# Kernel tuning notes

Hardware: AMD Instinct MI355X
Metric: run time of the kernel (lower is better)

The kernel has to match this reference:

```python
import jax, jax.numpy as jnp
import numpy as np

THRESHOLD = 0.5
SLACK = 3
EPS = 1e-12
B, H, W = 16, 512, 512


def _shift(p, dy, dx, b, h, w):
    # p is zero-padded by 1 on spatial dims; returns neighbor at offset (dy, dx)
    return p[:, 1 + dy:1 + dy + h, 1 + dx:1 + dx + w]


def _thin_sub(img, step):
    # One Zhang-Suen sub-iteration on bool image [B,H,W] (zero boundary, as skimage)
    b, h, w = img.shape
    p = jnp.pad(img.astype(jnp.int32), ((0, 0), (1, 1), (1, 1)))
    # P2..P9 clockwise starting at North
    P2 = _shift(p, -1, 0, b, h, w); P3 = _shift(p, -1, 1, b, h, w)
    P4 = _shift(p, 0, 1, b, h, w);  P5 = _shift(p, 1, 1, b, h, w)
    P6 = _shift(p, 1, 0, b, h, w);  P7 = _shift(p, 1, -1, b, h, w)
    P8 = _shift(p, 0, -1, b, h, w); P9 = _shift(p, -1, -1, b, h, w)
    seq = [P2, P3, P4, P5, P6, P7, P8, P9, P2]
    Bn = P2 + P3 + P4 + P5 + P6 + P7 + P8 + P9          # neighbor count
    A = sum((1 - seq[k]) * seq[k + 1] for k in range(8))  # 0->1 transitions
    cond = (Bn >= 2) & (Bn <= 6) & (A == 1)
    if step == 0:
        cond = cond & (P2 * P4 * P6 == 0) & (P4 * P6 * P8 == 0)
    else:
        cond = cond & (P2 * P4 * P8 == 0) & (P2 * P6 * P8 == 0)
    return img & ~cond


def _skeletonize(img):
    # Iterate Zhang-Suen thinning to convergence (skimage.morphology.skeletonize 2D = Zhang's method)
    def body(state):
        cur, _ = state
        nxt = _thin_sub(_thin_sub(cur, 0), 1)
        return (nxt, jnp.any(nxt != cur))

    out, _ = jax.lax.while_loop(lambda s: s[1], body, (img, jnp.array(True)))
    return out


def _edt_sq(mask):
    # Exact squared Euclidean distance to nearest True pixel, separable 2-pass.
    b, h, w = mask.shape
    BIG = h + w  # larger than any attainable 1D distance
    g = jnp.where(mask, 0, BIG).astype(jnp.int32)  # [B,H,W]

    # pass 1: 1D nearest-True distance along rows (axis=1) via fwd/bwd scans
    def fscan(carry, row):
        d = jnp.minimum(row, carry + 1)
        return d, d

    g_rows = jnp.moveaxis(g, 1, 0)  # [H,B,W]
    init = jnp.full((b, w), BIG, jnp.int32)
    _, fwd = jax.lax.scan(fscan, init, g_rows)
    _, bwd = jax.lax.scan(fscan, init, g_rows[::-1])
    f = jnp.minimum(jnp.minimum(fwd, bwd[::-1]), BIG)  # [H,B,W]
    f2 = jnp.moveaxis(f * f, 0, 1)  # [B,H,W] squared vertical distance

    # pass 2: d2[b,i,j] = min_{j'} f2[b,i,j'] + (j-j')^2 (lower envelope, memory-friendly lax.map)
    js = jnp.arange(w, dtype=jnp.int32)

    def one_col(j):
        off = (js - j) ** 2  # [W]
        return jnp.min(f2 + off[None, None, :], axis=-1)  # [B,H]

    d2 = jax.lax.map(one_col, js)  # [W,B,H]
    return jnp.transpose(d2, (1, 2, 0))  # [B,H,W]


def setup_inputs() -> dict:
    key = jax.random.key(0)
    k1, k2 = jax.random.split(key)
    y_pred = jax.random.uniform(k1, (B, H, W), dtype=jnp.float32)
    y_true = jax.random.uniform(k2, (B, H, W), dtype=jnp.float32)
    return {"y_pred": y_pred, "y_true": y_true}


def reference(y_pred, y_true):
    p = y_pred > THRESHOLD  # greater_is_road=True binarization
    g = y_true > THRESHOLD
    p = _skeletonize(p)
    g = _skeletonize(g)
    d2_gt = _edt_sq(g)   # EDT of ~g == distance to nearest g pixel
    d2_pr = _edt_sq(p)
    s2 = SLACK * SLACK   # dist <= slack  <=>  dist^2 <= slack^2 (integer sq EDT)
    tp_area = d2_gt <= s2
    fp_area = ~tp_area
    fn_area = d2_pr > s2
    ax = (1, 2)
    TP = jnp.sum(tp_area & p, ax).astype(jnp.float32)
    FP = jnp.sum(fp_area & p, ax).astype(jnp.float32)
    FN = jnp.sum(fn_area & g, ax).astype(jnp.float32)
    correctness = TP / (TP + FP + EPS)
    completeness = TP / (TP + FN + EPS)
    quality = TP / (TP + FP + FN + EPS)
    # mean over batch -> [3]: [correctness, completeness, quality]
    return jnp.mean(jnp.stack([correctness, completeness, quality], axis=1), axis=0)
```

## Files before the change

kernel.cpp:

```cpp
#include <hip/hip_runtime.h>
#include <stdint.h>

#define HH 512
#define WW 512
#define HW (HH * WW)
#define WPR 8
#define NWORDS (HH * WPR)
#define NTHREADS 1024
#define NB 16
#define NIMG (2 * NB)

#define LSTR 10
#define LROWS (HH + 2)
#define LWORDS (LROWS * LSTR)

typedef unsigned long long u64;

__device__ __forceinline__ u64 zs_core(u64 cc, u64 P2, u64 P3, u64 P4, u64 P5,
                                       u64 P6, u64 P7, u64 P8, u64 P9, int step) {
    u64 ab = P2 ^ P3;
    u64 s1 = ab ^ P4, c1 = (P2 & P3) | (ab & P4);
    u64 de = P5 ^ P6;
    u64 s2 = de ^ P7, c2 = (P5 & P6) | (de & P7);
    u64 s3 = P8 ^ P9, c3 = P8 & P9;
    u64 gh = s1 ^ s2;
    u64 b0 = gh ^ s3, c4 = (s1 & s2) | (gh & s3);
    u64 ij = c1 ^ c2;
    u64 s4 = ij ^ c3, c5 = (c1 & c2) | (ij & c3);
    u64 b1 = s4 ^ c4, c6 = s4 & c4;
    u64 b2 = c5 ^ c6, b3 = c5 & c6;

    u64 Bge2 = b1 | b2 | b3;
    u64 Ble6 = ~(b3 | (b2 & b1 & b0));

    u64 a1, a2, t;
    t = ~P2 & P3; a1 = t; a2 = 0ULL;
    t = ~P3 & P4; a2 |= a1 & t; a1 |= t;
    t = ~P4 & P5; a2 |= a1 & t; a1 |= t;
    t = ~P5 & P6; a2 |= a1 & t; a1 |= t;
    t = ~P6 & P7; a2 |= a1 & t; a1 |= t;
    t = ~P7 & P8; a2 |= a1 & t; a1 |= t;
    t = ~P8 & P9; a2 |= a1 & t; a1 |= t;
    t = ~P9 & P2; a2 |= a1 & t; a1 |= t;
    u64 Aeq1 = a1 & ~a2;

    u64 sccond = (step == 0) ? ~((P4 & P6) & (P2 | P8))
                             : ~((P2 & P8) & (P4 | P6));

    return cc & ~(Bge2 & Ble6 & Aeq1 & sccond);
}

__global__ __launch_bounds__(256)
void pack_kernel(const float* __restrict__ y_pred,
                 const float* __restrict__ y_true,
                 u64* __restrict__ bits ,
                 int* __restrict__ cnt ) {
    int tid = threadIdx.x;
    if (blockIdx.x == 0 && tid < 4 * NB + NIMG + 1) cnt[tid] = 0;

    int t = blockIdx.x * 256 + tid;
    size_t g0 = (size_t)t * 16;
    const float* src;
    size_t off;
    if (g0 < (size_t)NB * HW) { src = y_pred; off = g0; }
    else                      { src = y_true; off = g0 - (size_t)NB * HW; }
    const float4* s4 = (const float4*)(src + off);
    float4 a = s4[0];
    float4 b = s4[1];
    float4 c = s4[2];
    float4 d = s4[3];
    unsigned m =
        ((unsigned)(a.x > 0.5f) << 0)  | ((unsigned)(a.y > 0.5f) << 1)  |
        ((unsigned)(a.z > 0.5f) << 2)  | ((unsigned)(a.w > 0.5f) << 3)  |
        ((unsigned)(b.x > 0.5f) << 4)  | ((unsigned)(b.y > 0.5f) << 5)  |
        ((unsigned)(b.z > 0.5f) << 6)  | ((unsigned)(b.w > 0.5f) << 7)  |
        ((unsigned)(c.x > 0.5f) << 8)  | ((unsigned)(c.y > 0.5f) << 9)  |
        ((unsigned)(c.z > 0.5f) << 10) | ((unsigned)(c.w > 0.5f) << 11) |
        ((unsigned)(d.x > 0.5f) << 12) | ((unsigned)(d.y > 0.5f) << 13) |
        ((unsigned)(d.z > 0.5f) << 14) | ((unsigned)(d.w > 0.5f) << 15);
    ((unsigned short*)bits)[t] = (unsigned short)m;
}

#define SSTRIPS 8
#define SIROWS (HH / SSTRIPS)
#define SHALO 24
#define SDROWS (SIROWS + 2 * SHALO)
#define STHREADS (SDROWS * WPR)
#define SITERS (SHALO / 2)
#define SSTR 10
#define SLWORDS ((SDROWS + 2) * SSTR)

__global__ __launch_bounds__(STHREADS)
void strip_kernel(const u64* __restrict__ src, u64* __restrict__ dst,
                  int* __restrict__ flags, int rec) {
    __shared__ u64 Mb[2][SLWORDS];
    __shared__ int s_any[3];

    int bx = blockIdx.x;
    int img = bx >> 3;
    int s = bx & 7;
    int tid = threadIdx.x;
    int lane = tid & 63;
    int r = tid >> 3;
    int c = tid & 7;
    int gr = s * SIROWS - SHALO + r;

    for (int i = tid; i < SLWORDS; i += STHREADS) { Mb[0][i] = 0; Mb[1][i] = 0; }
    if (tid < 3) s_any[tid] = 0;
    __syncthreads();

    const u64* gsrc = src + (size_t)img * NWORDS;
    u64 v = (gr >= 0 && gr < HH) ? gsrc[gr * WPR + c] : 0ULL;
    int base = (r + 1) * SSTR + (c + 1);
    Mb[0][base] = v;

    bool prevchg = true;
    int it = 0;
    bool done = false;
    for (;;) {
        for (int step = 0; step < 2; ++step) {
            __syncthreads();
            if (step == 0 && it > 0) {
                if (s_any[(it + 2) % 3] == 0) { done = true; break; }
            }
            const u64* Ms = Mb[step];
            u64* Md = Mb[step ^ 1];
            u64 cc = Ms[base];
            u64 nv = cc;
            bool chg = false;
            if (cc) {
                u64 nm = Ms[base - SSTR - 1], nc = Ms[base - SSTR], np = Ms[base - SSTR + 1];
                u64 cm = Ms[base - 1],                              cp = Ms[base + 1];
                u64 sm = Ms[base + SSTR - 1], sc = Ms[base + SSTR], sp = Ms[base + SSTR + 1];
                u64 P2 = nc;
                u64 P3 = (nc >> 1) | (np << 63);
                u64 P4 = (cc >> 1) | (cp << 63);
                u64 P5 = (sc >> 1) | (sp << 63);
                u64 P6 = sc;
                u64 P7 = (sc << 1) | (sm >> 63);
                u64 P8 = (cc << 1) | (cm >> 63);
                u64 P9 = (nc << 1) | (nm >> 63);
                nv = zs_core(cc, P2, P3, P4, P5, P6, P7, P8, P9, step);
                chg = (nv != cc);
            }
            if (chg | prevchg) Md[base] = nv;
            prevchg = chg;
            u64 bal = __ballot(chg);
            if (bal && lane == 0) s_any[it % 3] = 1;
            if (step == 1 && tid == 0) s_any[(it + 1) % 3] = 0;
        }
        if (done) break;
        if (++it >= SITERS) break;
    }
    __syncthreads();
    int lastAny = done ? 0 : s_any[(SITERS - 1) % 3];

    if (r >= SHALO && r < SHALO + SIROWS) {
        dst[(size_t)img * NWORDS + gr * WPR + c] = Mb[0][base];
    }
    if (rec && lastAny && tid == 0) flags[img] = 1;
}

__global__ __launch_bounds__(NTHREADS, 4)
void skel_kernel(u64* __restrict__ bits, const int* __restrict__ flags) {
    __shared__ u64 Mb[2][LWORDS];
    __shared__ unsigned int Cpb[2][130];
    __shared__ int s_any[3];

    int bx = blockIdx.x;
    if (flags[bx] == 0) return;

    int tid = threadIdx.x;
    int lane = tid & 63;
    int c = tid & 7;
    int rb = tid >> 3;

    u64* gm = bits + (size_t)bx * NWORDS;

    if (tid < LROWS) {
        int i = tid;
        if (i == 0 || i == LROWS - 1) {
            #pragma unroll
            for (int j = 0; j < LSTR; ++j) { Mb[0][i * LSTR + j] = 0; Mb[1][i * LSTR + j] = 0; }
        } else {
            Mb[0][i * LSTR + 0] = 0; Mb[0][i * LSTR + 9] = 0;
            Mb[1][i * LSTR + 0] = 0; Mb[1][i * LSTR + 9] = 0;
        }
    }
    {
        const ulonglong2* s2 = (const ulonglong2*)gm;
        #pragma unroll
        for (int k = 0; k < 2; ++k) {
            int i = k * NTHREADS + tid;
            ulonglong2 v = s2[i];
            int wi = i * 2;
            int r = wi >> 3, c2 = wi & 7;
            int li = (r + 1) * LSTR + c2 + 1;
            Mb[0][li] = v.x;
            Mb[0][li + 1] = v.y;
        }
    }
    if (tid < 130) {
        Cpb[0][tid] = (tid >= 1 && tid <= 128) ? 0x1FEu : 0u;
        Cpb[1][tid] = 0u;
    }
    if (tid < 3) s_any[tid] = 0;

    unsigned dl = 0x1FEu;
    bool prevchg = true;
    int base = (rb * 4 + 1) * LSTR + (c + 1);

    int it = 0;
    bool done = false;
    for (;;) {
        for (int step = 0; step < 2; ++step) {
            __syncthreads();
            if (step == 0 && it > 0) {
                if (s_any[(it + 2) % 3] == 0) { done = true; break; }
            }
            const u64* Ms = Mb[step];
            u64* Md = Mb[step ^ 1];
            const unsigned* CpS = Cpb[step];
            unsigned* CpD = Cpb[step ^ 1];

            unsigned need = ((CpS[rb] | CpS[rb + 1] | CpS[rb + 2]) >> c) & 7u;
            bool chg = false;
            if (need) {
                u64 Ca, Ea, Wa, Cb, Eb, Wb, Cc, Ec, Wc;
                {   int a = base - LSTR;
                    u64 x = Ms[a], mm = Ms[a - 1], pp = Ms[a + 1];
                    Ca = x; Ea = (x >> 1) | (pp << 63); Wa = (x << 1) | (mm >> 63); }
                {   int a = base;
                    u64 x = Ms[a], mm = Ms[a - 1], pp = Ms[a + 1];
                    Cb = x; Eb = (x >> 1) | (pp << 63); Wb = (x << 1) | (mm >> 63); }
                u64 nv0 = 0, nv1 = 0, nv2 = 0, nv3 = 0;
                {   int a = base + LSTR;
                    u64 x = Ms[a], mm = Ms[a - 1], pp = Ms[a + 1];
                    Cc = x; Ec = (x >> 1) | (pp << 63); Wc = (x << 1) | (mm >> 63);
                    if (Cb) nv0 = zs_core(Cb, Ca, Ea, Eb, Ec, Cc, Wc, Wb, Wa, step);
                    chg |= (nv0 != Cb);
                    Ca = Cb; Ea = Eb; Wa = Wb; Cb = Cc; Eb = Ec; Wb = Wc; }
                {   int a = base + 2 * LSTR;
                    u64 x = Ms[a], mm = Ms[a - 1], pp = Ms[a + 1];
                    Cc = x; Ec = (x >> 1) | (pp << 63); Wc = (x << 1) | (mm >> 63);
                    if (Cb) nv1 = zs_core(Cb, Ca, Ea, Eb, Ec, Cc, Wc, Wb, Wa, step);
                    chg |= (nv1 != Cb);
                    Ca = Cb; Ea = Eb; Wa = Wb; Cb = Cc; Eb = Ec; Wb = Wc; }
                {   int a = base + 3 * LSTR;
                    u64 x = Ms[a], mm = Ms[a - 1], pp = Ms[a + 1];
                    Cc = x; Ec = (x >> 1) | (pp << 63); Wc = (x << 1) | (mm >> 63);
                    if (Cb) nv2 = zs_core(Cb, Ca, Ea, Eb, Ec, Cc, Wc, Wb, Wa, step);
                    chg |= (nv2 != Cb);
                    Ca = Cb; Ea = Eb; Wa = Wb; Cb = Cc; Eb = Ec; Wb = Wc; }
                {   int a = base + 4 * LSTR;
                    u64 x = Ms[a], mm = Ms[a - 1], pp = Ms[a + 1];
                    Cc = x; Ec = (x >> 1) | (pp << 63); Wc = (x << 1) | (mm >> 63);
                    if (Cb) nv3 = zs_core(Cb, Ca, Ea, Eb, Ec, Cc, Wc, Wb, Wa, step);
                    chg |= (nv3 != Cb); }
                if (chg | prevchg) {
                    Md[base] = nv0;
                    Md[base + LSTR] = nv1;
                    Md[base + 2 * LSTR] = nv2;
                    Md[base + 3 * LSTR] = nv3;
                }
            }
            prevchg = chg;
            u64 bal = __ballot(chg);
            if (bal && lane == 0) s_any[it % 3] = 1;
            if ((lane & 7) == 0) {
                unsigned byte = ((unsigned)(bal >> lane) & 0xFFu) << 1;
                CpD[rb + 1] = byte | dl;
                dl = byte;
            }
            if (step == 1 && tid == 0) s_any[(it + 1) % 3] = 0;
        }
        if (done || it >= 1024) break;
        ++it;
    }

    {
        ulonglong2* d2 = (ulonglong2*)gm;
        #pragma unroll
        for (int k = 0; k < 2; ++k) {
            int i = k * NTHREADS + tid;
            int wi = i * 2;
            int r = wi >> 3, c2 = wi & 7;
            int li = (r + 1) * LSTR + c2 + 1;
            ulonglong2 v;
            v.x = Mb[0][li];
            v.y = Mb[0][li + 1];
            d2[i] = v;
        }
    }
}

#define STRIPS 8
#define SROWS (HH / STRIPS)
#define SR2 (SROWS + 6)

__device__ __forceinline__ u64 ldws(const u64* M, int r, int c) {
    return (c < 0 || c >= WPR) ? 0ULL : M[r * WPR + c];
}

__device__ __forceinline__ u64 dil3s(const u64* M, int r, int c) {
    u64 cm = ldws(M, r, c - 1), cc = ldws(M, r, c), cp = ldws(M, r, c + 1);
    u64 h = cc
          | (cc >> 1) | (cp << 63)
          | (cc >> 2) | (cp << 62)
          | (cc >> 3) | (cp << 61)
          | (cc << 1) | (cm >> 63)
          | (cc << 2) | (cm >> 62)
          | (cc << 3) | (cm >> 61);
    u64 um = ldws(M, r - 1, c - 1) | ldws(M, r + 1, c - 1) | ldws(M, r - 2, c - 1) | ldws(M, r + 2, c - 1);
    u64 uc = ldws(M, r - 1, c    ) | ldws(M, r + 1, c    ) | ldws(M, r - 2, c    ) | ldws(M, r + 2, c    );
    u64 up = ldws(M, r - 1, c + 1) | ldws(M, r + 1, c + 1) | ldws(M, r - 2, c + 1) | ldws(M, r + 2, c + 1);
    h |= uc
       | (uc >> 1) | (up << 63)
       | (uc >> 2) | (up << 62)
       | (uc << 1) | (um >> 63)
       | (uc << 2) | (um >> 62);
    h |= ldws(M, r - 3, c) | ldws(M, r + 3, c);
    return h;
}

__global__ __launch_bounds__(256)
void count_kernel(const u64* __restrict__ skel, int* __restrict__ cnt,
                  int* __restrict__ done, float* __restrict__ out) {
    __shared__ u64 P[SR2 * WPR];
    __shared__ u64 G[SR2 * WPR];
    __shared__ int acc[4];
    __shared__ int s_last;

    int b = blockIdx.x / STRIPS;
    int s = blockIdx.x % STRIPS;
    int tid = threadIdx.x;
    int r0 = s * SROWS - 3;

    const u64* sp = skel + (size_t)b * NWORDS;
    const u64* sg = skel + (size_t)(NB + b) * NWORDS;
    for (int i = tid; i < SR2 * WPR; i += 256) {
        int gr = r0 + (i >> 3);
        bool in = (gr >= 0 && gr < HH);
        int gi = gr * WPR + (i & 7);
        P[i] = in ? sp[gi] : 0ULL;
        G[i] = in ? sg[gi] : 0ULL;
    }
    if (tid < 4) acc[tid] = 0;
    __syncthreads();

    int cp = 0, cg = 0, tp = 0, fnh = 0;
    #pragma unroll
    for (int k = 0; k < 2; ++k) {
        int w = k * 256 + tid;
        int r = (w >> 3) + 3, c = w & 7;
        u64 pw = P[r * WPR + c], gw = G[r * WPR + c];
        cp  += __popcll(pw);
        cg  += __popcll(gw);
        tp  += __popcll(pw & dil3s(G, r, c));
        fnh += __popcll(gw & dil3s(P, r, c));
    }
    #pragma unroll
    for (int o = 32; o > 0; o >>= 1) {
        cp  += __shfl_down(cp, o);
        cg  += __shfl_down(cg, o);
        tp  += __shfl_down(tp, o);
        fnh += __shfl_down(fnh, o);
    }
    if ((tid & 63) == 0) {
        atomicAdd(&acc[0], cp);
        atomicAdd(&acc[1], cg);
        atomicAdd(&acc[2], tp);
        atomicAdd(&acc[3], fnh);
    }
    __syncthreads();
    if (tid < 4) atomicAdd(&cnt[b * 4 + tid], acc[tid]);
    __syncthreads();
    if (tid == 0) {
        __threadfence();
        s_last = (atomicAdd(done, 1) == NB * STRIPS - 1);
    }
    __syncthreads();
    if (!s_last) return;
    __threadfence();

    if (tid < 3) {
        float sacc = 0.0f;
        for (int i = 0; i < NB; ++i) {
            float c0 = (float)atomicAdd(&cnt[i * 4 + 0], 0);
            float c1 = (float)atomicAdd(&cnt[i * 4 + 1], 0);
            float TP = (float)atomicAdd(&cnt[i * 4 + 2], 0);
            float c3 = (float)atomicAdd(&cnt[i * 4 + 3], 0);
            float FP = c0 - TP;
            float FN = c1 - c3;
            float v = (tid == 0) ? TP / (TP + FP + 1e-12f)
                    : (tid == 1) ? TP / (TP + FN + 1e-12f)
                                 : TP / (TP + FP + FN + 1e-12f);
            sacc += v;
        }
        out[tid] = sacc * (1.0f / NB);
    }
}

extern "C" void kernel_launch(void* const* d_in, const int* in_sizes, int n_in,
                              void* d_out, int out_size, void* d_ws, size_t ws_size,
                              hipStream_t stream) {
    (void)in_sizes; (void)n_in; (void)out_size; (void)ws_size;
    const float* y_pred = (const float*)d_in[0];
    const float* y_true = (const float*)d_in[1];
    float* out = (float*)d_out;

    u64* buf1 = (u64*)d_ws;
    u64* buf2 = buf1 + (size_t)NIMG * NWORDS;
    int* cnt = (int*)(buf2 + (size_t)NIMG * NWORDS);
    int* flags = cnt + 4 * NB;
    int* done = flags + NIMG;

    hipLaunchKernelGGL(pack_kernel, dim3(2 * NB * HW / 16 / 256), dim3(256), 0, stream,
                       y_pred, y_true, buf1, cnt);
    hipLaunchKernelGGL(strip_kernel, dim3(NIMG * SSTRIPS), dim3(STHREADS), 0, stream,
                       buf1, buf2, flags, 0);
    hipLaunchKernelGGL(strip_kernel, dim3(NIMG * SSTRIPS), dim3(STHREADS), 0, stream,
                       buf2, buf1, flags, 1);
    hipLaunchKernelGGL(skel_kernel, dim3(NIMG), dim3(NTHREADS), 0, stream,
                       buf1, flags);
    hipLaunchKernelGGL(count_kernel, dim3(NB * STRIPS), dim3(256), 0, stream,
                       buf1, cnt, done, out);
}
```

Measured before the change: 117.9 us.

## Pack bits via wave ballots and skip inactive words in strip thinning

The pack kernel now has each thread load one float4 and assembles 64-bit words with four wave ballots plus bit spreading, replacing the per-thread 16-float loads and 16-bit stores. The strip kernel keeps per-row change masks in shared memory, double-buffered across steps. A word is recomputed only if it or a neighbouring word changed in the previous step, which skips shared loads and logic for settled regions. This adds ballot, shared-memory bookkeeping and a delayed-mask scheme whose correctness relies on tracking changes across two sub-iterations.

Result: faster. 112.6 us (-4.5%).

```diff
diff --git a/kernel.cpp b/kernel.cpp
--- a/kernel.cpp
+++ b/kernel.cpp
@@ -50,6 +50,14 @@
     return cc & ~(Bge2 & Ble6 & Aeq1 & sccond);
 }
 
+__device__ __forceinline__ u64 spread4(u64 x) {
+    x = (x | (x << 24)) & 0x000000FF000000FFULL;
+    x = (x | (x << 12)) & 0x000F000F000F000FULL;
+    x = (x | (x << 6))  & 0x0303030303030303ULL;
+    x = (x | (x << 3))  & 0x1111111111111111ULL;
+    return x;
+}
+
 __global__ __launch_bounds__(256)
 void pack_kernel(const float* __restrict__ y_pred,
                  const float* __restrict__ y_true,
@@ -59,26 +67,30 @@
     if (blockIdx.x == 0 && tid < 4 * NB + NIMG + 1) cnt[tid] = 0;
 
     int t = blockIdx.x * 256 + tid;
-    size_t g0 = (size_t)t * 16;
+    int lane = tid & 63;
+    size_t p0 = (size_t)t * 4;
     const float* src;
     size_t off;
-    if (g0 < (size_t)NB * HW) { src = y_pred; off = g0; }
-    else                      { src = y_true; off = g0 - (size_t)NB * HW; }
-    const float4* s4 = (const float4*)(src + off);
-    float4 a = s4[0];
-    float4 b = s4[1];
-    float4 c = s4[2];
-    float4 d = s4[3];
-    unsigned m =
-        ((unsigned)(a.x > 0.5f) << 0)  | ((unsigned)(a.y > 0.5f) << 1)  |
-        ((unsigned)(a.z > 0.5f) << 2)  | ((unsigned)(a.w > 0.5f) << 3)  |
-        ((unsigned)(b.x > 0.5f) << 4)  | ((unsigned)(b.y > 0.5f) << 5)  |
-        ((unsigned)(b.z > 0.5f) << 6)  | ((unsigned)(b.w > 0.5f) << 7)  |
-        ((unsigned)(c.x > 0.5f) << 8)  | ((unsigned)(c.y > 0.5f) << 9)  |
-        ((unsigned)(c.z > 0.5f) << 10) | ((unsigned)(c.w > 0.5f) << 11) |
-        ((unsigned)(d.x > 0.5f) << 12) | ((unsigned)(d.y > 0.5f) << 13) |
-        ((unsigned)(d.z > 0.5f) << 14) | ((unsigned)(d.w > 0.5f) << 15);
-    ((unsigned short*)bits)[t] = (unsigned short)m;
+    if (p0 < (size_t)NB * HW) { src = y_pred; off = p0; }
+    else                      { src = y_true; off = p0 - (size_t)NB * HW; }
+    float4 a = *(const float4*)(src + off);
+    unsigned nib = (unsigned)(a.x > 0.5f)
+                 | ((unsigned)(a.y > 0.5f) << 1)
+                 | ((unsigned)(a.z > 0.5f) << 2)
+                 | ((unsigned)(a.w > 0.5f) << 3);
+    u64 b0 = __ballot(nib & 1u);
+    u64 b1 = __ballot(nib & 2u);
+    u64 b2 = __ballot(nib & 4u);
+    u64 b3 = __ballot(nib & 8u);
+    if (lane < 4) {
+        unsigned sh = lane * 16;
+        u64 w = spread4((b0 >> sh) & 0xFFFFu)
+              | (spread4((b1 >> sh) & 0xFFFFu) << 1)
+              | (spread4((b2 >> sh) & 0xFFFFu) << 2)
+              | (spread4((b3 >> sh) & 0xFFFFu) << 3);
+        size_t wave = (size_t)t >> 6;
+        bits[wave * 4 + lane] = w;
+    }
 }
 
 #define SSTRIPS 8
@@ -94,6 +106,7 @@
 void strip_kernel(const u64* __restrict__ src, u64* __restrict__ dst,
                   int* __restrict__ flags, int rec) {
     __shared__ u64 Mb[2][SLWORDS];
+    __shared__ unsigned int Cpb[2][SDROWS + 2];
     __shared__ int s_any[3];
 
     int bx = blockIdx.x;
@@ -106,6 +119,10 @@
     int gr = s * SIROWS - SHALO + r;
 
     for (int i = tid; i < SLWORDS; i += STHREADS) { Mb[0][i] = 0; Mb[1][i] = 0; }
+    if (tid < SDROWS + 2) {
+        Cpb[0][tid] = (tid >= 1 && tid <= SDROWS) ? 0x1FEu : 0u;
+        Cpb[1][tid] = 0u;
+    }
     if (tid < 3) s_any[tid] = 0;
     __syncthreads();
 
@@ -114,6 +131,7 @@
     int base = (r + 1) * SSTR + (c + 1);
     Mb[0][base] = v;
 
+    unsigned dl = 0x1FEu;
     bool prevchg = true;
     int it = 0;
     bool done = false;
@@ -125,28 +143,39 @@
             }
             const u64* Ms = Mb[step];
             u64* Md = Mb[step ^ 1];
-            u64 cc = Ms[base];
-            u64 nv = cc;
+            const unsigned* CpS = Cpb[step];
+            unsigned* CpD = Cpb[step ^ 1];
+
+            unsigned need = ((CpS[r] | CpS[r + 1] | CpS[r + 2]) >> c) & 7u;
             bool chg = false;
-            if (cc) {
-                u64 nm = Ms[base - SSTR - 1], nc = Ms[base - SSTR], np = Ms[base - SSTR + 1];
-                u64 cm = Ms[base - 1],                              cp = Ms[base + 1];
-                u64 sm = Ms[base + SSTR - 1], sc = Ms[base + SSTR], sp = Ms[base + SSTR + 1];
-                u64 P2 = nc;
-                u64 P3 = (nc >> 1) | (np << 63);
-                u64 P4 = (cc >> 1) | (cp << 63);
-                u64 P5 = (sc >> 1) | (sp << 63);
-                u64 P6 = sc;
-                u64 P7 = (sc << 1) | (sm >> 63);
-                u64 P8 = (cc << 1) | (cm >> 63);
-                u64 P9 = (nc << 1) | (nm >> 63);
-                nv = zs_core(cc, P2, P3, P4, P5, P6, P7, P8, P9, step);
-                chg = (nv != cc);
-            }
-            if (chg | prevchg) Md[base] = nv;
+            if (need) {
+                u64 cc = Ms[base];
+                u64 nv = cc;
+                if (cc) {
+                    u64 nm = Ms[base - SSTR - 1], nc = Ms[base - SSTR], np = Ms[base - SSTR + 1];
+                    u64 cm = Ms[base - 1],                              cp = Ms[base + 1];
+                    u64 sm = Ms[base + SSTR - 1], sc = Ms[base + SSTR], sp = Ms[base + SSTR + 1];
+                    u64 P2 = nc;
+                    u64 P3 = (nc >> 1) | (np << 63);
+                    u64 P4 = (cc >> 1) | (cp << 63);
+                    u64 P5 = (sc >> 1) | (sp << 63);
+                    u64 P6 = sc;
+                    u64 P7 = (sc << 1) | (sm >> 63);
+                    u64 P8 = (cc << 1) | (cm >> 63);
+                    u64 P9 = (nc << 1) | (nm >> 63);
+                    nv = zs_core(cc, P2, P3, P4, P5, P6, P7, P8, P9, step);
+                    chg = (nv != cc);
+                }
+                if (chg | prevchg) Md[base] = nv;
+            }
             prevchg = chg;
             u64 bal = __ballot(chg);
             if (bal && lane == 0) s_any[it % 3] = 1;
+            if ((lane & 7) == 0) {
+                unsigned byte = ((unsigned)(bal >> lane) & 0xFFu) << 1;
+                CpD[r + 1] = byte | dl;
+                dl = byte;
+            }
             if (step == 1 && tid == 0) s_any[(it + 1) % 3] = 0;
         }
         if (done) break;
@@ -415,7 +444,7 @@
     int* flags = cnt + 4 * NB;
     int* done = flags + NIMG;
 
-    hipLaunchKernelGGL(pack_kernel, dim3(2 * NB * HW / 16 / 256), dim3(256), 0, stream,
+    hipLaunchKernelGGL(pack_kernel, dim3(2 * NB * HW / 4 / 256), dim3(256), 0, stream,
                        y_pred, y_true, buf1, cnt);
     hipLaunchKernelGGL(strip_kernel, dim3(NIMG * SSTRIPS), dim3(STHREADS), 0, stream,
                        buf1, buf2, flags, 0);
```
